# Kernel optimization log

Measured on AMD Instinct MI355X. Metric: run time of the kernel, lower is better.

## Reference

```python
import jax, jax.numpy as jnp
import numpy as np

BATCHING_INFO = {0: {'max_tokens': 16, 'batching_range': (0, 16)},
                 1: {'max_tokens': 32, 'batching_range': (16, 32)},
                 2: {'max_tokens': 48, 'batching_range': (32, 100000)}}
WINDOW_SHAPE = (10, 10, 4)
SPARSE_SHAPE = (400, 400, 16)
POS_TEMPERATURE = 1000.0
N_VOXELS = 300000
FEAT_DIM = 192


def get_window_coors_np(coors, sparse_shape, window_shape, do_shift):
    wx, wy, wz = window_shape
    sx, sy, sz = sparse_shape
    mx = int(np.ceil(sx / wx) + 1)
    my = int(np.ceil(sy / wy) + 1)
    mz = int(np.ceil(sz / wz) + 1)
    mper = mx * my * mz
    if do_shift:
        shx, shy, shz = wx // 2, wy // 2, wz // 2
    else:
        shx, shy, shz = wx, wy, wz
    if wz == sz:
        shz = 0
    scx = coors[:, 3] + shx
    scy = coors[:, 2] + shy
    scz = coors[:, 1] + shz
    wcx = scx // wx
    wcy = scy // wy
    wcz = scz // wz
    batch_win_inds = coors[:, 0] * mper + wcx * my * mz + wcy * mz + wcz
    coors_in_win = np.stack([scz % wz, scy % wy, scx % wx], axis=-1)
    return batch_win_inds, coors_in_win


def get_inner_win_inds_np(win_inds):
    # rank of each voxel within its window, stable w.r.t. original order
    n = len(win_inds)
    order = np.argsort(win_inds, kind='stable')
    sw = win_inds[order]
    starts = np.r_[0, np.flatnonzero(np.diff(sw)) + 1]
    counts = np.diff(np.r_[starts, n])
    ranks = np.arange(n) - np.repeat(starts, counts)
    inner = np.empty(n, dtype=np.int64)
    inner[order] = ranks
    return inner


def batching_single_shift(batch_win_inds):
    lvl = -np.ones_like(batch_win_inds)
    inner = get_inner_win_inds_np(batch_win_inds)
    bincount = np.bincount(batch_win_inds)
    num_before = bincount[batch_win_inds]
    target = np.zeros_like(batch_win_inds)
    for bl, info in BATCHING_INFO.items():
        lo, hi = info['batching_range']
        m = (num_before >= lo) & (num_before < hi)
        target[m] = info['max_tokens']
        lvl[m] = bl
    return inner < target, lvl


def get_flat2win_inds_np(batch_win_inds, lvl):
    d = {}
    for dl, info in BATCHING_INFO.items():
        m = lvl == dl
        if not m.any():
            continue
        sub = batch_win_inds[m]
        uniq, conti = np.unique(sub, return_inverse=True)
        inner = get_inner_win_inds_np(sub)
        d[dl] = (conti * info['max_tokens'] + inner, np.flatnonzero(m), len(uniq))
    d['voxel_batching_level'] = lvl
    return d


def partition_indices(coors):
    # full window partition + two-shift voxel batching (pure int logic)
    bwi0, ciw0 = get_window_coors_np(coors, SPARSE_SHAPE, WINDOW_SHAPE, False)
    bwi1, ciw1 = get_window_coors_np(coors, SPARSE_SHAPE, WINDOW_SHAPE, True)
    keep0, lvl0 = batching_single_shift(bwi0)
    idx = np.flatnonzero(keep0)
    lvl0 = lvl0[keep0]
    bwi0 = bwi0[keep0]
    bwi1k = bwi1[keep0]
    keep1, lvl1 = batching_single_shift(bwi1k)
    idx = idx[keep1]
    lvl0 = lvl0[keep1]
    bwi0 = bwi0[keep1]
    lvl1 = lvl1[keep1]
    bwi1k = bwi1k[keep1]
    inds0 = get_flat2win_inds_np(bwi0, lvl0)
    inds1 = get_flat2win_inds_np(bwi1k, lvl1)
    return idx, ciw0[idx], ciw1[idx], inds0, inds1


def get_pos_embed(coors_in_win, feat_dim):
    wx, wy, wz = WINDOW_SHAPE
    c = jnp.asarray(coors_in_win, jnp.float32)
    z = c[:, 0] - wz / 2.0
    y = c[:, 1] - wy / 2.0
    x = c[:, 2] - wx / 2.0
    pos_length = feat_dim // 3
    i = jnp.arange(pos_length, dtype=jnp.float32)
    inv_freq = jnp.power(jnp.float32(POS_TEMPERATURE), 2.0 * jnp.floor(i / 2.0) / pos_length)

    def emb(v):
        e = v[:, None] / inv_freq[None, :]
        return jnp.stack([jnp.sin(e[:, ::2]), jnp.cos(e[:, 1::2])], axis=-1).reshape(e.shape[0], -1)

    return jnp.concatenate([emb(x), emb(y), emb(z)], axis=-1)


def flat2window(feat, inds_dict):
    out = {}
    for dl in sorted(k for k in inds_dict if isinstance(k, int)):
        flat_inds, pos, nwin = inds_dict[dl]
        T = BATCHING_INFO[dl]['max_tokens']
        buf = jnp.zeros((nwin * T, feat.shape[-1]), feat.dtype)
        buf = buf.at[jnp.asarray(flat_inds)].set(feat[jnp.asarray(pos)])
        out[dl] = buf.reshape(nwin, T, feat.shape[-1])
    return out


def setup_inputs() -> dict:
    key = jax.random.key(0)
    rng = np.random.default_rng(0)
    b = rng.integers(0, 2, N_VOXELS)
    z = rng.integers(0, SPARSE_SHAPE[2], N_VOXELS)
    y = rng.integers(0, SPARSE_SHAPE[1], N_VOXELS)
    x = rng.integers(0, SPARSE_SHAPE[0], N_VOXELS)
    coords = np.stack([b, z, y, x], axis=1).astype(np.int64)
    feats = jax.random.normal(key, (N_VOXELS, FEAT_DIM), jnp.float32)
    return {'voxel_features': feats, 'voxel_coords': jnp.asarray(coords)}


def reference(voxel_features, voxel_coords):
    coors = np.asarray(voxel_coords)
    idx, ciw0, ciw1, inds0, inds1 = partition_indices(coors)
    idx_j = jnp.asarray(idx)
    feats = voxel_features[idx_j]
    coords_kept = jnp.asarray(coors[idx])
    outs = [feats, coords_kept]
    for ciw, inds in ((ciw0, inds0), (ciw1, inds1)):
        pe = get_pos_embed(ciw, voxel_features.shape[1])
        pe_dict = flat2window(pe, inds)
        for dl in sorted(k for k in inds if isinstance(k, int)):
            outs.append(pe_dict[dl])
        for dl in sorted(k for k in inds if isinstance(k, int)):
            flat_inds, pos, nwin = inds[dl]
            T = BATCHING_INFO[dl]['max_tokens']
            filled = jnp.zeros((nwin * T,), bool).at[jnp.asarray(flat_inds)].set(True)
            outs.append(jnp.logical_not(filled).reshape(nwin, T))  # key_padding_mask
    return tuple(outs)
```

## Files before the change

kernel.cpp:

```cpp
#include <hip/hip_runtime.h>
#include <math.h>

typedef unsigned int u32;
typedef unsigned short u16;

#define WTOT 16810
#define MPER 8405
#define MAXROWS (WTOT * 48)

#define M_NKEPT 0
#define M_NWIN0 1
#define M_NWIN1 4
#define M_WORDS 16

__device__ __forceinline__ int level_of(int c) {
    if (c < 16) return 0;
    if (c < 32) return 1;
    return 2;
}
__device__ __forceinline__ int target_of(int lvl) {
    return (lvl == 0) ? 16 : ((lvl == 1) ? 32 : 48);
}

__device__ __forceinline__ int wave_incl_scan(int v) {
#pragma unroll
    for (int o = 1; o < 64; o <<= 1) {
        int t = __shfl_up(v, o, 64);
        if ((int)(threadIdx.x & 63) >= o) v += t;
    }
    return v;
}

__device__ __forceinline__ int block_incl_scan_1024(int v, int* wsums, int* total) {
    int lane = threadIdx.x & 63, wid = threadIdx.x >> 6;
    int iv = wave_incl_scan(v);
    if (lane == 63) wsums[wid] = iv;
    __syncthreads();
    if (wid == 0) {
        int s = (lane < 16) ? wsums[lane] : 0;
        s = wave_incl_scan(s);
        if (lane < 16) wsums[lane] = s;
    }
    __syncthreads();
    int add = (wid > 0) ? wsums[wid - 1] : 0;
    int incl = iv + add;
    *total = wsums[15];
    __syncthreads();
    return incl;
}

__device__ __forceinline__ int block_is64(const int* c32, int* sh) {
    if (threadIdx.x < 64) {
        unsigned long long b = __ballot(c32[2 * threadIdx.x + 1] != 0);
        if (threadIdx.x == 0) *sh = (b == 0ULL) ? 1 : 0;
    }
    __syncthreads();
    return *sh;
}


__global__ __launch_bounds__(256) void k_wincoords(const void* coors_raw, int N, int NB,
        int CE2, int* bwi0, int* bwi1, int* ciw0, int* ciw1, u32* H0, float* dict) {
    __shared__ int s64;
    if ((int)blockIdx.x >= NB) {
        int e = ((int)blockIdx.x - NB) * 256 + (int)threadIdx.x;
        if (e < 76800) {
            int idx = e / 192;
            int j = e - idx * 192;
            int dz = idx & 3;
            int dy = (idx >> 2) % 10;
            int dx = (idx >> 2) / 10;
            int sel = j >> 6;
            float v = (sel == 0) ? ((float)dx - 5.0f)
                    : ((sel == 1) ? ((float)dy - 5.0f) : ((float)dz - 2.0f));
            int kk = (j & 63) >> 1;
            float invf = (float)exp(6.907755278982137 * (double)kk / 32.0);
            float a = v / invf;
            dict[e] = (j & 1) ? cosf(a) : sinf(a);
        }
        return;
    }
    int is64 = block_is64((const int*)coors_raw, &s64);
    int i = (int)blockIdx.x * 256 + (int)threadIdx.x;
    if (i >= N) return;
    int b, z, y, x;
    if (is64) {
        const long long* c = (const long long*)coors_raw;
        long long o = 4LL * i;
        b = (int)c[o]; z = (int)c[o + 1]; y = (int)c[o + 2]; x = (int)c[o + 3];
    } else {
        const int* c = (const int*)coors_raw;
        b = c[4 * i]; z = c[4 * i + 1]; y = c[4 * i + 2]; x = c[4 * i + 3];
    }
    int ch = i >> 10;
    {
        int scx = x + 10, scy = y + 10, scz = z + 4;
        int w = b * MPER + (scx / 10) * 205 + (scy / 10) * 5 + (scz >> 2);
        bwi0[i] = w;
        ciw0[i] = (scz & 3) | ((scy % 10) << 8) | ((scx % 10) << 16);
        atomicAdd(&H0[(size_t)w * CE2 + (ch >> 1)], 1u << ((ch & 1) * 16));
    }
    {
        int scx = x + 5, scy = y + 5, scz = z + 2;
        int w = b * MPER + (scx / 10) * 205 + (scy / 10) * 5 + (scz >> 2);
        bwi1[i] = w;
        ciw1[i] = (scz & 3) | ((scy % 10) << 8) | ((scx % 10) << 16);
    }
}

__global__ __launch_bounds__(256) void k_prefix16(u32* H, u16* counts, int CE2, int NW) {
    int w = ((int)blockIdx.x * 256 + (int)threadIdx.x) >> 6;
    int lane = threadIdx.x & 63;
    if (w >= NW) return;
    u32* row = H + (size_t)w * CE2;
    u32 run = 0;
    for (int p0 = 0; p0 < CE2; p0 += 64) {
        int p = p0 + lane;
        u32 v = (p < CE2) ? row[p] : 0u;
        u32 lo = v & 0xffffu, hi = v >> 16;
        int s = (int)(lo + hi);
        int incl = wave_incl_scan(s);
        u32 excl = (u32)(incl - s);
        u32 offlo = run + excl;
        u32 offhi = offlo + lo;
        if (offlo > 1023u) offlo = 1023u;
        if (offhi > 1023u) offhi = 1023u;
        if (p < CE2) row[p] = offlo | (offhi << 16);
        int tot = __shfl(incl, 63, 64);
        run += (u32)tot;
        if (run > 1023u) run = 1023u;
    }
    if (lane == 0) counts[w] = (u16)run;
}

__global__ __launch_bounds__(1024) void k_stage1(const int* bwi0, const int* bwi1,
        const u16* counts0, const u16* H0_16, u32* H1, int* keep0, int N, int CE, int CE2) {
    __shared__ alignas(16) int swin[1024];
    int c = blockIdx.x, t = threadIdx.x;
    int i = (c << 10) + t;
    int w0 = (i < N) ? bwi0[i] : -1;
    swin[t] = w0;
    __syncthreads();
    if (i >= N) return;
    int local = 0;
    int jlim = ((t >> 6) + 1) << 6;
    const int4* s4 = (const int4*)swin;
    for (int j = 0; j < jlim; j += 4) {
        int4 q = s4[j >> 2];
        local += (q.x == w0 && j + 0 < t);
        local += (q.y == w0 && j + 1 < t);
        local += (q.z == w0 && j + 2 < t);
        local += (q.w == w0 && j + 3 < t);
    }
    int inner = (int)H0_16[(size_t)w0 * CE + c] + local;
    int k0 = inner < target_of(level_of((int)counts0[w0]));
    keep0[i] = k0;
    if (k0) atomicAdd(&H1[(size_t)bwi1[i] * CE2 + (c >> 1)], 1u << ((c & 1) * 16));
}

__global__ __launch_bounds__(1024) void k_stage2(const int* bwi0, const int* bwi1,
        const int* keep0, const u16* counts1k, const u16* H1_16,
        u32* HF0, u32* HF1, int* keepf, int* chunkcnt, int N, int CE, int CE2) {
    __shared__ alignas(16) int swin[1024];
    __shared__ int blksum;
    int c = blockIdx.x, t = threadIdx.x;
    int i = (c << 10) + t;
    int k0 = (i < N) ? keep0[i] : 0;
    int w1 = k0 ? bwi1[i] : -1;
    swin[t] = w1;
    if (t == 0) blksum = 0;
    __syncthreads();
    int kf = 0;
    if (w1 >= 0) {
        int local = 0;
        int jlim = ((t >> 6) + 1) << 6;
        const int4* s4 = (const int4*)swin;
        for (int j = 0; j < jlim; j += 4) {
            int4 q = s4[j >> 2];
            local += (q.x == w1 && j + 0 < t);
            local += (q.y == w1 && j + 1 < t);
            local += (q.z == w1 && j + 2 < t);
            local += (q.w == w1 && j + 3 < t);
        }
        int inner1 = (int)H1_16[(size_t)w1 * CE + c] + local;
        kf = inner1 < target_of(level_of((int)counts1k[w1]));
    }
    if (i < N) keepf[i] = kf;
    if (kf) {
        int w0 = bwi0[i];
        atomicAdd(&HF0[(size_t)w0 * CE2 + (c >> 1)], 1u << ((c & 1) * 16));
        atomicAdd(&HF1[(size_t)w1 * CE2 + (c >> 1)], 1u << ((c & 1) * 16));
    }
    unsigned long long b = __ballot(kf);
    if ((t & 63) == 0) atomicAdd(&blksum, __popcll(b));
    __syncthreads();
    if (t == 0) chunkcnt[c] = blksum;
}

__global__ __launch_bounds__(1024) void k_midscan(int* chunkcnt, int C, int* meta,
        const u16* counts0, const u16* fcount0, int* conti0,
        const u16* counts1, const u16* fcount1, int* conti1) {
    __shared__ int wsums[16];
    __shared__ int running;
    __shared__ int run3[3];
    if (blockIdx.x == 0) {
        if (threadIdx.x == 0) running = 0;
        __syncthreads();
        for (int base = 0; base < C; base += 1024) {
            int i = base + threadIdx.x;
            int v = (i < C) ? chunkcnt[i] : 0;
            int total;
            int incl = block_incl_scan_1024(v, wsums, &total);
            int run = running;
            if (i < C) chunkcnt[i] = run + incl - v;
            __syncthreads();
            if (threadIdx.x == 0) running = run + total;
            __syncthreads();
        }
        if (threadIdx.x == 0) meta[M_NKEPT] = running;
    } else {
        const u16* counts = (blockIdx.x == 2) ? counts1 : counts0;
        const u16* fcount = (blockIdx.x == 2) ? fcount1 : fcount0;
        int* conti = (blockIdx.x == 2) ? conti1 : conti0;
        int* nwin_out = meta + ((blockIdx.x == 2) ? M_NWIN1 : M_NWIN0);
        if (threadIdx.x < 3) run3[threadIdx.x] = 0;
        __syncthreads();
        for (int base = 0; base < WTOT; base += 1024) {
            int i = base + threadIdx.x;
            int c = (i < WTOT) ? (int)counts[i] : 0;
            int f = (i < WTOT) ? (int)fcount[i] : 0;
            int lvl = level_of(c);
            int act = (c > 0 && f > 0) ? 1 : 0;
            int packed = act ? (1 << (11 * lvl)) : 0;
            int total;
            int incl = block_incl_scan_1024(packed, wsums, &total);
            int excl = incl - packed;
            int r0 = run3[0], r1 = run3[1], r2 = run3[2];
            if (i < WTOT) {
                int e;
                if (lvl == 0) e = r0 + (excl & 2047);
                else if (lvl == 1) e = r1 + ((excl >> 11) & 2047);
                else e = r2 + ((excl >> 22) & 2047);
                conti[i] = e;
            }
            __syncthreads();
            if (threadIdx.x == 0) {
                run3[0] = r0 + (total & 2047);
                run3[1] = r1 + ((total >> 11) & 2047);
                run3[2] = r2 + ((total >> 22) & 2047);
            }
            __syncthreads();
        }
        if (threadIdx.x < 3) nwin_out[threadIdx.x] = run3[threadIdx.x];
    }
}

__global__ __launch_bounds__(1024) void k_stage3(const int* bwi0, const int* bwi1,
        const int* ciw0, const int* ciw1, const int* keepf,
        const u16* counts0, const u16* counts1k,
        const int* conti0, const int* conti1,
        const u16* HF0_16, const u16* HF1_16, const int* chunkpref,
        const int* meta, int* idxarr, int* rowvox0, int* rowvox1, int N, int CE) {
    __shared__ alignas(16) int sw0[1024];
    __shared__ alignas(16) int sw1[1024];
    int c = blockIdx.x, t = threadIdx.x;
    int i = (c << 10) + t;
    int kf = (i < N) ? keepf[i] : 0;
    int w0 = kf ? bwi0[i] : -1;
    int w1 = kf ? bwi1[i] : -1;
    sw0[t] = w0;
    sw1[t] = w1;
    __syncthreads();
    if (!kf) return;
    int l0 = 0, l1 = 0, lk = 0;
    int jlim = ((t >> 6) + 1) << 6;
    const int4* a4 = (const int4*)sw0;
    const int4* b4 = (const int4*)sw1;
    for (int j = 0; j < jlim; j += 4) {
        int4 qa = a4[j >> 2];
        int4 qb = b4[j >> 2];
        int v0 = (j + 0 < t), v1 = (j + 1 < t), v2 = (j + 2 < t), v3 = (j + 3 < t);
        l0 += (qa.x == w0 && v0) + (qa.y == w0 && v1) + (qa.z == w0 && v2) + (qa.w == w0 && v3);
        lk += (qa.x != -1 && v0) + (qa.y != -1 && v1) + (qa.z != -1 && v2) + (qa.w != -1 && v3);
        l1 += (qb.x == w1 && v0) + (qb.y == w1 && v1) + (qb.z == w1 && v2) + (qb.w == w1 && v3);
    }
    int innerF0 = (int)HF0_16[(size_t)w0 * CE + c] + l0;
    int innerF1 = (int)HF1_16[(size_t)w1 * CE + c] + l1;
    int kpos = chunkpref[c] + lk;
    idxarr[kpos] = i;
    int n00 = meta[M_NWIN0], n01 = meta[M_NWIN0 + 1];
    int n10 = meta[M_NWIN1], n11 = meta[M_NWIN1 + 1];
    {
        int lvl = level_of((int)counts0[w0]);
        int T = target_of(lvl);
        int rb = (lvl == 0) ? 0 : ((lvl == 1) ? n00 * 16 : (n00 * 16 + n01 * 32));
        rowvox0[rb + conti0[w0] * T + innerF0] = ciw0[i];
    }
    {
        int lvl = level_of((int)counts1k[w1]);
        int T = target_of(lvl);
        int rb = (lvl == 0) ? 0 : ((lvl == 1) ? n10 * 16 : (n10 * 16 + n11 * 32));
        rowvox1[rb + conti1[w1] * T + innerF1] = ciw1[i];
    }
}

__global__ __launch_bounds__(256) void k_render(const float* feats, const void* coors_raw,
        const int* meta, const int* idxarr, const int* rowvox0, const int* rowvox1,
        const float* dict, float* out, int NA) {
    __shared__ int s64;
    int nk = meta[M_NKEPT];
    int n00 = meta[M_NWIN0], n01 = meta[M_NWIN0 + 1], n02 = meta[M_NWIN0 + 2];
    int n10 = meta[M_NWIN1], n11 = meta[M_NWIN1 + 1], n12 = meta[M_NWIN1 + 2];
    int R0 = n00 * 16 + n01 * 32 + n02 * 48;
    int R1 = n10 * 16 + n11 * 32 + n12 * 48;
    int obuf0 = nk * 196;
    int omask0 = obuf0 + R0 * 192;
    int obuf1 = omask0 + R0;
    int omask1 = obuf1 + R1 * 192;
    int ototal = omask1 + R1;
    if ((int)blockIdx.x < NA) {
        int is64 = block_is64((const int*)coors_raw, &s64);
        int ocoor = nk * 192;
        const float4* src = (const float4*)feats;
        float4* dst = (float4*)out;
        int tot = nk * 52;
        int step = NA * 256;
        for (int idx = (int)blockIdx.x * 256 + (int)threadIdx.x; idx < tot; idx += step) {
            if (idx < nk * 48) {
                int row = idx / 48;
                int col = idx - row * 48;
                dst[idx] = src[(size_t)idxarr[row] * 48 + col];
            } else {
                int cidx = idx - nk * 48;
                int k = cidx >> 2, tt = cidx & 3;
                int ii = idxarr[k];
                int v = is64 ? (int)((const long long*)coors_raw)[4LL * ii + tt]
                             : ((const int*)coors_raw)[4 * ii + tt];
                out[ocoor + cidx] = (float)v;
            }
        }
    } else {
        int q0 = obuf0 >> 2, q1 = ototal >> 2;
        const float4* dict4 = (const float4*)dict;
        float4* out4 = (float4*)out;
        int step = ((int)gridDim.x - NA) * 256;
        for (int q = q0 + ((int)blockIdx.x - NA) * 256 + (int)threadIdx.x; q < q1; q += step) {
            int e = q << 2;
            float4 val;
            bool pe1 = (e >= obuf1) && (e < omask1);
            if ((e < omask0) || pe1) {
                unsigned rel = (unsigned)(e - (pe1 ? obuf1 : obuf0));
                unsigned row = rel / 192u;
                unsigned j = rel - row * 192u;
                int ciw = pe1 ? rowvox1[row] : rowvox0[row];
                if (ciw < 0) {
                    val.x = val.y = val.z = val.w = 0.0f;
                } else {
                    int di = (ciw & 3) + ((ciw >> 8) & 15) * 4 + ((ciw >> 16) & 15) * 40;
                    val = dict4[di * 48 + (int)(j >> 2)];
                }
            } else {
                int base = (e >= omask1) ? omask1 : omask0;
                const int* rv = (e >= omask1) ? rowvox1 : rowvox0;
                int4 c4 = *(const int4*)(rv + (e - base));
                val.x = (c4.x < 0) ? 1.0f : 0.0f;
                val.y = (c4.y < 0) ? 1.0f : 0.0f;
                val.z = (c4.z < 0) ? 1.0f : 0.0f;
                val.w = (c4.w < 0) ? 1.0f : 0.0f;
            }
            out4[q] = val;
        }
    }
}

extern "C" void kernel_launch(void* const* d_in, const int* in_sizes, int n_in,
                              void* d_out, int out_size, void* d_ws, size_t ws_size,
                              hipStream_t stream) {
    const float* feats = (const float*)d_in[0];
    const void* coors = d_in[1];
    int N = in_sizes[0] / 192;
    int C = (N + 1023) >> 10;
    int CE = (C + 1) & ~1;
    int CE2 = CE >> 1;
    size_t TW32 = (size_t)WTOT * CE2;
    int N4 = (N + 3) & ~3;

    u32* U = (u32*)d_ws;
    int* bwi0 = (int*)U;            int* bwi1 = bwi0 + N4;
    int* ciw0 = bwi1 + N4;          int* ciw1 = ciw0 + N4;
    int* keep0 = ciw1 + N4;         int* keepf = keep0 + N4;
    int* idxarr = keepf + N4;
    u32* H0 = (u32*)(idxarr + N4);
    u32* H1 = H0 + TW32;
    u32* HF0 = H1 + TW32;
    u32* HF1 = HF0 + TW32;
    u16* counts0 = (u16*)(HF1 + TW32);
    u16* counts1k = (u16*)((u32*)counts0 + 8408);
    u16* fcount0 = (u16*)((u32*)counts1k + 8408);
    u16* fcount1 = fcount0 + WTOT;
    int* chunkcnt = (int*)((u32*)fcount0 + 16812);
    int CP4 = (C + 3) & ~3;
    int* conti0 = chunkcnt + CP4;
    int* conti1 = conti0 + 16812;
    int* rowvox0 = conti1 + 16812;
    int* rowvox1 = rowvox0 + MAXROWS;
    int* meta = rowvox1 + MAXROWS;
    float* dict = (float*)(meta + M_WORDS);

    int nb256 = (N + 255) / 256;

    hipMemsetAsync(H0, 0, 4 * TW32 * sizeof(u32), stream);
    hipMemsetAsync(rowvox0, 0xFF, (size_t)2 * MAXROWS * sizeof(int), stream);

    k_wincoords<<<nb256 + 300, 256, 0, stream>>>(coors, N, nb256, CE2,
                                                 bwi0, bwi1, ciw0, ciw1, H0, dict);

    int pgrid = (WTOT * 64 + 255) / 256;
    k_prefix16<<<pgrid, 256, 0, stream>>>(H0, counts0, CE2, WTOT);
    k_stage1<<<C, 1024, 0, stream>>>(bwi0, bwi1, counts0, (const u16*)H0, H1, keep0, N, CE, CE2);

    k_prefix16<<<pgrid, 256, 0, stream>>>(H1, counts1k, CE2, WTOT);
    k_stage2<<<C, 1024, 0, stream>>>(bwi0, bwi1, keep0, counts1k, (const u16*)H1,
                                     HF0, HF1, keepf, chunkcnt, N, CE, CE2);

    k_prefix16<<<2 * pgrid, 256, 0, stream>>>(HF0, fcount0, CE2, 2 * WTOT);
    k_midscan<<<3, 1024, 0, stream>>>(chunkcnt, C, meta,
                                      counts0, fcount0, conti0,
                                      counts1k, fcount1, conti1);

    k_stage3<<<C, 1024, 0, stream>>>(bwi0, bwi1, ciw0, ciw1, keepf, counts0, counts1k,
                                     conti0, conti1, (const u16*)HF0, (const u16*)HF1,
                                     chunkcnt, meta, idxarr, rowvox0, rowvox1, N, CE);

    k_render<<<4096, 256, 0, stream>>>(feats, coors, meta, idxarr, rowvox0, rowvox1,
                                       dict, (float*)d_out, 1536);

    (void)n_in; (void)ws_size; (void)out_size;
}
```

Measured before the change: 1.284 ms.

## Rank in-chunk duplicates via compact shared lists and use nontemporal output stores

Stages 1-3 no longer do an O(t) scan over all earlier threads' window ids to find each voxel's in-chunk rank. Each thread reads the per-chunk histogram prefix and the next entry to get its window's count in this chunk. Only voxels whose window has two or more members in the chunk are appended to a compact shared list, and only those threads scan that list. Stage3 computes the kept-voxel prefix with a ballot/popcount wave scan instead of the loop, and the render kernel writes output with nontemporal stores. This cuts shared-memory scanning work but adds shared atomics and extra syncs, and the list order is nondeterministic, which is harmless because rank uses the thread-id bits.

```diff
diff --git a/kernel.cpp b/kernel.cpp
--- a/kernel.cpp
+++ b/kernel.cpp
@@ -3,6 +3,7 @@
 
 typedef unsigned int u32;
 typedef unsigned short u16;
+typedef __attribute__((ext_vector_type(4))) float f32x4;
 
 #define WTOT 16810
 #define MPER 8405
@@ -56,6 +57,20 @@
     }
     __syncthreads();
     return *sh;
+}
+
+__device__ __forceinline__ int list_rank(const u32* list, int lcount, u32 key, int t) {
+    int local = 0;
+    int L4 = (lcount + 3) >> 2;
+    const uint4* l4 = (const uint4*)list;
+    for (int p = 0; p < L4; p++) {
+        uint4 e = l4[p];
+        local += ((e.x & ~1023u) == key && (int)(e.x & 1023u) < t);
+        local += ((e.y & ~1023u) == key && (int)(e.y & 1023u) < t);
+        local += ((e.z & ~1023u) == key && (int)(e.z & 1023u) < t);
+        local += ((e.w & ~1023u) == key && (int)(e.w & 1023u) < t);
+    }
+    return local;
 }
 
 
@@ -135,25 +150,27 @@
 
 __global__ __launch_bounds__(1024) void k_stage1(const int* bwi0, const int* bwi1,
         const u16* counts0, const u16* H0_16, u32* H1, int* keep0, int N, int CE, int CE2) {
-    __shared__ alignas(16) int swin[1024];
+    __shared__ alignas(16) u32 list[1028];
+    __shared__ int lcount;
     int c = blockIdx.x, t = threadIdx.x;
     int i = (c << 10) + t;
-    int w0 = (i < N) ? bwi0[i] : -1;
-    swin[t] = w0;
+    if (t == 0) lcount = 0;
+    __syncthreads();
+    int w0 = -1, cur = 0, cnt = 0;
+    if (i < N) {
+        w0 = bwi0[i];
+        size_t ro = (size_t)w0 * CE + c;
+        cur = (int)H0_16[ro];
+        int nxt = (c + 1 < CE) ? (int)H0_16[ro + 1] : (int)counts0[w0];
+        cnt = nxt - cur;
+        if (cnt >= 2) { int p = atomicAdd(&lcount, 1); list[p] = ((u32)w0 << 10) | (u32)t; }
+    }
+    __syncthreads();
+    if (t < 3) list[lcount + t] = 0xFFFFFFFFu;
     __syncthreads();
     if (i >= N) return;
-    int local = 0;
-    int jlim = ((t >> 6) + 1) << 6;
-    const int4* s4 = (const int4*)swin;
-    for (int j = 0; j < jlim; j += 4) {
-        int4 q = s4[j >> 2];
-        local += (q.x == w0 && j + 0 < t);
-        local += (q.y == w0 && j + 1 < t);
-        local += (q.z == w0 && j + 2 < t);
-        local += (q.w == w0 && j + 3 < t);
-    }
-    int inner = (int)H0_16[(size_t)w0 * CE + c] + local;
-    int k0 = inner < target_of(level_of((int)counts0[w0]));
+    int local = (cnt >= 2) ? list_rank(list, lcount, (u32)w0 << 10, t) : 0;
+    int k0 = (cur + local) < target_of(level_of((int)counts0[w0]));
     keep0[i] = k0;
     if (k0) atomicAdd(&H1[(size_t)bwi1[i] * CE2 + (c >> 1)], 1u << ((c & 1) * 16));
 }
@@ -161,34 +178,33 @@
 __global__ __launch_bounds__(1024) void k_stage2(const int* bwi0, const int* bwi1,
         const int* keep0, const u16* counts1k, const u16* H1_16,
         u32* HF0, u32* HF1, int* keepf, int* chunkcnt, int N, int CE, int CE2) {
-    __shared__ alignas(16) int swin[1024];
-    __shared__ int blksum;
+    __shared__ alignas(16) u32 list[1028];
+    __shared__ int lcount, blksum;
     int c = blockIdx.x, t = threadIdx.x;
     int i = (c << 10) + t;
     int k0 = (i < N) ? keep0[i] : 0;
-    int w1 = k0 ? bwi1[i] : -1;
-    swin[t] = w1;
-    if (t == 0) blksum = 0;
+    if (t == 0) { lcount = 0; blksum = 0; }
+    __syncthreads();
+    int w1 = -1, cur = 0, cnt = 0;
+    if (k0) {
+        w1 = bwi1[i];
+        size_t ro = (size_t)w1 * CE + c;
+        cur = (int)H1_16[ro];
+        int nxt = (c + 1 < CE) ? (int)H1_16[ro + 1] : (int)counts1k[w1];
+        cnt = nxt - cur;
+        if (cnt >= 2) { int p = atomicAdd(&lcount, 1); list[p] = ((u32)w1 << 10) | (u32)t; }
+    }
+    __syncthreads();
+    if (t < 3) list[lcount + t] = 0xFFFFFFFFu;
     __syncthreads();
     int kf = 0;
-    if (w1 >= 0) {
-        int local = 0;
-        int jlim = ((t >> 6) + 1) << 6;
-        const int4* s4 = (const int4*)swin;
-        for (int j = 0; j < jlim; j += 4) {
-            int4 q = s4[j >> 2];
-            local += (q.x == w1 && j + 0 < t);
-            local += (q.y == w1 && j + 1 < t);
-            local += (q.z == w1 && j + 2 < t);
-            local += (q.w == w1 && j + 3 < t);
-        }
-        int inner1 = (int)H1_16[(size_t)w1 * CE + c] + local;
-        kf = inner1 < target_of(level_of((int)counts1k[w1]));
+    if (k0) {
+        int local = (cnt >= 2) ? list_rank(list, lcount, (u32)w1 << 10, t) : 0;
+        kf = (cur + local) < target_of(level_of((int)counts1k[w1]));
     }
     if (i < N) keepf[i] = kf;
     if (kf) {
-        int w0 = bwi0[i];
-        atomicAdd(&HF0[(size_t)w0 * CE2 + (c >> 1)], 1u << ((c & 1) * 16));
+        atomicAdd(&HF0[(size_t)bwi0[i] * CE2 + (c >> 1)], 1u << ((c & 1) * 16));
         atomicAdd(&HF1[(size_t)w1 * CE2 + (c >> 1)], 1u << ((c & 1) * 16));
     }
     unsigned long long b = __ballot(kf);
@@ -259,35 +275,50 @@
         const int* ciw0, const int* ciw1, const int* keepf,
         const u16* counts0, const u16* counts1k,
         const int* conti0, const int* conti1,
-        const u16* HF0_16, const u16* HF1_16, const int* chunkpref,
-        const int* meta, int* idxarr, int* rowvox0, int* rowvox1, int N, int CE) {
-    __shared__ alignas(16) int sw0[1024];
-    __shared__ alignas(16) int sw1[1024];
-    int c = blockIdx.x, t = threadIdx.x;
+        const u16* HF0_16, const u16* HF1_16,
+        const u16* fcount0, const u16* fcount1,
+        const int* chunkpref, const int* meta,
+        int* idxarr, int* rowvox0, int* rowvox1, int N, int CE) {
+    __shared__ alignas(16) u32 list0[1028];
+    __shared__ alignas(16) u32 list1[1028];
+    __shared__ int lc0, lc1, wsum[16];
+    int c = blockIdx.x, t = threadIdx.x, lane = t & 63, wv = t >> 6;
     int i = (c << 10) + t;
+    if (t == 0) { lc0 = 0; lc1 = 0; }
     int kf = (i < N) ? keepf[i] : 0;
-    int w0 = kf ? bwi0[i] : -1;
-    int w1 = kf ? bwi1[i] : -1;
-    sw0[t] = w0;
-    sw1[t] = w1;
+    unsigned long long m = __ballot(kf);
+    if (lane == 0) wsum[wv] = __popcll(m);
+    __syncthreads();
+    if (t < 64) {
+        int s = (t < 16) ? wsum[t] : 0;
+        s = wave_incl_scan(s);
+        if (t < 16) wsum[t] = s;
+    }
+    __syncthreads();
+    int lk = (wv ? wsum[wv - 1] : 0) + __popcll(m & ((1ull << lane) - 1ull));
+    int w0 = -1, w1 = -1, cur0 = 0, cur1 = 0, cnt0 = 0, cnt1 = 0;
+    if (kf) {
+        w0 = bwi0[i]; w1 = bwi1[i];
+        size_t r0o = (size_t)w0 * CE + c;
+        cur0 = (int)HF0_16[r0o];
+        int nxt0 = (c + 1 < CE) ? (int)HF0_16[r0o + 1] : (int)fcount0[w0];
+        cnt0 = nxt0 - cur0;
+        if (cnt0 >= 2) { int p = atomicAdd(&lc0, 1); list0[p] = ((u32)w0 << 10) | (u32)t; }
+        size_t r1o = (size_t)w1 * CE + c;
+        cur1 = (int)HF1_16[r1o];
+        int nxt1 = (c + 1 < CE) ? (int)HF1_16[r1o + 1] : (int)fcount1[w1];
+        cnt1 = nxt1 - cur1;
+        if (cnt1 >= 2) { int p = atomicAdd(&lc1, 1); list1[p] = ((u32)w1 << 10) | (u32)t; }
+    }
+    __syncthreads();
+    if (t < 3) { list0[lc0 + t] = 0xFFFFFFFFu; list1[lc1 + t] = 0xFFFFFFFFu; }
     __syncthreads();
     if (!kf) return;
-    int l0 = 0, l1 = 0, lk = 0;
-    int jlim = ((t >> 6) + 1) << 6;
-    const int4* a4 = (const int4*)sw0;
-    const int4* b4 = (const int4*)sw1;
-    for (int j = 0; j < jlim; j += 4) {
-        int4 qa = a4[j >> 2];
-        int4 qb = b4[j >> 2];
-        int v0 = (j + 0 < t), v1 = (j + 1 < t), v2 = (j + 2 < t), v3 = (j + 3 < t);
-        l0 += (qa.x == w0 && v0) + (qa.y == w0 && v1) + (qa.z == w0 && v2) + (qa.w == w0 && v3);
-        lk += (qa.x != -1 && v0) + (qa.y != -1 && v1) + (qa.z != -1 && v2) + (qa.w != -1 && v3);
-        l1 += (qb.x == w1 && v0) + (qb.y == w1 && v1) + (qb.z == w1 && v2) + (qb.w == w1 && v3);
-    }
-    int innerF0 = (int)HF0_16[(size_t)w0 * CE + c] + l0;
-    int innerF1 = (int)HF1_16[(size_t)w1 * CE + c] + l1;
-    int kpos = chunkpref[c] + lk;
-    idxarr[kpos] = i;
+    int l0 = (cnt0 >= 2) ? list_rank(list0, lc0, (u32)w0 << 10, t) : 0;
+    int l1 = (cnt1 >= 2) ? list_rank(list1, lc1, (u32)w1 << 10, t) : 0;
+    int innerF0 = cur0 + l0;
+    int innerF1 = cur1 + l1;
+    idxarr[chunkpref[c] + lk] = i;
     int n00 = meta[M_NWIN0], n01 = meta[M_NWIN0 + 1];
     int n10 = meta[M_NWIN1], n11 = meta[M_NWIN1 + 1];
     {
@@ -321,15 +352,16 @@
     if ((int)blockIdx.x < NA) {
         int is64 = block_is64((const int*)coors_raw, &s64);
         int ocoor = nk * 192;
-        const float4* src = (const float4*)feats;
-        float4* dst = (float4*)out;
+        const f32x4* src = (const f32x4*)feats;
+        f32x4* dst = (f32x4*)out;
         int tot = nk * 52;
         int step = NA * 256;
         for (int idx = (int)blockIdx.x * 256 + (int)threadIdx.x; idx < tot; idx += step) {
             if (idx < nk * 48) {
                 int row = idx / 48;
                 int col = idx - row * 48;
-                dst[idx] = src[(size_t)idxarr[row] * 48 + col];
+                f32x4 v = src[(size_t)idxarr[row] * 48 + col];
+                __builtin_nontemporal_store(v, dst + idx);
             } else {
                 int cidx = idx - nk * 48;
                 int k = cidx >> 2, tt = cidx & 3;
@@ -341,12 +373,12 @@
         }
     } else {
         int q0 = obuf0 >> 2, q1 = ototal >> 2;
-        const float4* dict4 = (const float4*)dict;
-        float4* out4 = (float4*)out;
+        const f32x4* dict4 = (const f32x4*)dict;
+        f32x4* out4 = (f32x4*)out;
         int step = ((int)gridDim.x - NA) * 256;
         for (int q = q0 + ((int)blockIdx.x - NA) * 256 + (int)threadIdx.x; q < q1; q += step) {
             int e = q << 2;
-            float4 val;
+            f32x4 val;
             bool pe1 = (e >= obuf1) && (e < omask1);
             if ((e < omask0) || pe1) {
                 unsigned rel = (unsigned)(e - (pe1 ? obuf1 : obuf0));
@@ -354,7 +386,7 @@
                 unsigned j = rel - row * 192u;
                 int ciw = pe1 ? rowvox1[row] : rowvox0[row];
                 if (ciw < 0) {
-                    val.x = val.y = val.z = val.w = 0.0f;
+                    val = (f32x4){0.0f, 0.0f, 0.0f, 0.0f};
                 } else {
                     int di = (ciw & 3) + ((ciw >> 8) & 15) * 4 + ((ciw >> 16) & 15) * 40;
                     val = dict4[di * 48 + (int)(j >> 2)];
@@ -368,7 +400,7 @@
                 val.z = (c4.z < 0) ? 1.0f : 0.0f;
                 val.w = (c4.w < 0) ? 1.0f : 0.0f;
             }
-            out4[q] = val;
+            __builtin_nontemporal_store(val, out4 + q);
         }
     }
 }
@@ -430,7 +462,8 @@
 
     k_stage3<<<C, 1024, 0, stream>>>(bwi0, bwi1, ciw0, ciw1, keepf, counts0, counts1k,
                                      conti0, conti1, (const u16*)HF0, (const u16*)HF1,
-                                     chunkcnt, meta, idxarr, rowvox0, rowvox1, N, CE);
+                                     fcount0, fcount1, chunkcnt, meta,
+                                     idxarr, rowvox0, rowvox1, N, CE);
 
     k_render<<<4096, 256, 0, stream>>>(feats, coors, meta, idxarr, rowvox0, rowvox1,
                                        dict, (float*)d_out, 1536);
```

New measurement: 1.193 ms. 1.08x faster.
